# Kernel optimization log

Hardware: AMD Instinct MI355X
Metric: run time of the kernel (lower is better)

Reference implementation:

```python
import jax, jax.numpy as jnp
import numpy as np

NUM_ITERATIONS = 3


def squash(x, axis):
    # squared_norm/(1+squared_norm) * x / sqrt(squared_norm), as in the torch module
    sn = jnp.sum(x * x, axis=axis, keepdims=True)
    return sn / (1.0 + sn) * x / jnp.sqrt(sn)


def setup_inputs() -> dict:
    key = jax.random.key(0)
    k1, k2 = jax.random.split(key)
    batch, num_caps, num_route, in_ch, out_ch = 32, 32, 4608, 8, 16
    x = jax.random.normal(k1, (batch, num_route, in_ch), dtype=jnp.float32)
    route_weights = jax.random.normal(k2, (num_caps, num_route, in_ch, out_ch), dtype=jnp.float32)
    return {"x": x, "route_weights": route_weights}


def reference(x, route_weights):
    # U[b,c,r,1,o] = x[b,1,r,1,i] @ W[1,c,r,i,o]
    U = jnp.einsum("bri,crio->bcro", x, route_weights)[:, :, :, None, :]  # [b,c,r,1,o]
    B = jnp.zeros_like(U)
    V = None
    for _ in range(NUM_ITERATIONS):
        C = jax.nn.softmax(B, axis=1)                 # softmax over capsules
        S = jnp.sum(C * U, axis=2, keepdims=True)      # reduce over route nodes: [b,c,1,1,o]
        V = squash(S, axis=-1)
        B = B + U * V
    b, c = B.shape[0], B.shape[1]
    o = B.shape[-1]
    return V.reshape(b, c, o)
```

## Files before the change

kernel.cpp:

```cpp
#include <hip/hip_runtime.h>

#define BATCH 32
#define NCAPS 32
#define NR    4608
#define NI    8
#define NO    16
#define CSTR  200
#define MAXRB 36
#define NCH   256
#define L2E   1.44269504088896341f

typedef float f2 __attribute__((ext_vector_type(2)));
typedef _Float16 half4v __attribute__((ext_vector_type(4)));
typedef _Float16 half8v __attribute__((ext_vector_type(8)));

template<int RB>
__global__ __launch_bounds__(1024, 2) void caps_route_store(
    const float* __restrict__ x,
    const float* __restrict__ W,
    float* __restrict__ P,
    unsigned short* __restrict__ Uh)
{
    constexpr int NP = RB / 2;
    __shared__ __align__(16) float Ws[2][2][NCAPS * CSTR];
    __shared__ __align__(16) f2    xP[RB][8][2][NI];

    const int t  = threadIdx.x;
    const int om = (t & 3) | (((t >> 3) & 1) << 2);
    const int co = ((t >> 4) & 1) | (((t >> 2) & 1) << 1) | (((t >> 5) & 1) << 2);
    const int w  = t >> 6;
    const int oh = w & 1;
    const int bq = w >> 1;
    const int o  = oh * 8 + om;
    const int b0 = 4 * bq;
    const int r0 = blockIdx.x * RB;

    f2 acc[2][4];
#pragma unroll
    for (int p = 0; p < 2; ++p)
#pragma unroll
        for (int cl = 0; cl < 4; ++cl) acc[p][cl] = (f2)0.f;

    for (int s = t; s < RB * 16; s += 1024) {
        const int rr = s >> 4, bp = s & 15;
        const float* xp0 = &x[((size_t)(2 * bp + 0) * NR + r0 + rr) * NI];
        const float* xp1 = &x[((size_t)(2 * bp + 1) * NR + r0 + rr) * NI];
        const float4 a0 = *(const float4*)xp0;
        const float4 a1 = *(const float4*)(xp0 + 4);
        const float4 c0 = *(const float4*)xp1;
        const float4 c1 = *(const float4*)(xp1 + 4);
        f2* d = &xP[rr][bp >> 1][bp & 1][0];
        d[0] = f2{a0.x, c0.x}; d[1] = f2{a0.y, c0.y};
        d[2] = f2{a0.z, c0.z}; d[3] = f2{a0.w, c0.w};
        d[4] = f2{a1.x, c1.x}; d[5] = f2{a1.y, c1.y};
        d[6] = f2{a1.z, c1.z}; d[7] = f2{a1.w, c1.w};
    }

    const int c_st = t >> 5;
    const int sl   = (c_st >> 2) + 8 * (c_st & 3);
    const int part = t & 31;
    const int i_st = part >> 2;
    const int o0   = (part & 3) * 4;
    const int dst  = sl * CSTR + o0 * 12 + i_st;
    const float* wsrc = W + ((size_t)c_st * NR + r0) * (NI * NO) + part * 4;

    {
        const float4 s0 = *(const float4*)wsrc;
        const float4 s1 = *(const float4*)(wsrc + NI * NO);
        float* d0 = &Ws[0][0][dst];
        d0[0] = s0.x; d0[12] = s0.y; d0[24] = s0.z; d0[36] = s0.w;
        float* d1 = &Ws[0][1][dst];
        d1[0] = s1.x; d1[12] = s1.y; d1[24] = s1.z; d1[36] = s1.w;
    }
    float4 pfa = {}, pfb = {};
    if (NP > 1) {
        pfa = *(const float4*)(wsrc + 2 * NI * NO);
        pfb = *(const float4*)(wsrc + 3 * NI * NO);
    }
    __syncthreads();

    auto compute_store = [&](const float* wt, const f2* xv, int r) {
        f2 xq[2][NI];
#pragma unroll
        for (int i = 0; i < NI; ++i) { xq[0][i] = xv[i]; xq[1][i] = xv[NI + i]; }
        const float* wb = wt + co * CSTR + o * 12;
        f2 u[2][4];
#pragma unroll
        for (int cl = 0; cl < 4; ++cl) {
            const float* wp = wb + cl * (8 * CSTR);
            const float4 w0 = *(const float4*)wp;
            const float4 w1 = *(const float4*)(wp + 4);
#pragma unroll
            for (int p = 0; p < 2; ++p) {
                f2 u2 = xq[p][0] * w0.x;
                u2 += xq[p][1] * w0.y;
                u2 += xq[p][2] * w0.z;
                u2 += xq[p][3] * w0.w;
                u2 += xq[p][4] * w1.x;
                u2 += xq[p][5] * w1.y;
                u2 += xq[p][6] * w1.z;
                u2 += xq[p][7] * w1.w;
                u[p][cl] = u2;
                acc[p][cl] += u2;
            }
        }
        unsigned short* ub = Uh + (((size_t)r * BATCH + b0) * NO + o) * NCAPS + 4 * co;
#pragma unroll
        for (int bb = 0; bb < 4; ++bb) {
            const int p = bb >> 1, h = bb & 1;
            half4v hv;
            hv[0] = (_Float16)(h ? u[p][0].y : u[p][0].x);
            hv[1] = (_Float16)(h ? u[p][1].y : u[p][1].x);
            hv[2] = (_Float16)(h ? u[p][2].y : u[p][2].x);
            hv[3] = (_Float16)(h ? u[p][3].y : u[p][3].x);
            *(half4v*)(ub + (size_t)bb * (NO * NCAPS)) = hv;
        }
    };

#pragma unroll 1
    for (int rp = 0; rp < NP; ++rp) {
        const int cur = rp & 1;
        if (rp + 1 < NP) {
            float* d0 = &Ws[cur ^ 1][0][dst];
            d0[0] = pfa.x; d0[12] = pfa.y; d0[24] = pfa.z; d0[36] = pfa.w;
            float* d1 = &Ws[cur ^ 1][1][dst];
            d1[0] = pfb.x; d1[12] = pfb.y; d1[24] = pfb.z; d1[36] = pfb.w;
            if (rp + 2 < NP) {
                pfa = *(const float4*)(wsrc + (size_t)(2 * rp + 4) * (NI * NO));
                pfb = *(const float4*)(wsrc + (size_t)(2 * rp + 5) * (NI * NO));
            }
        }
        compute_store(&Ws[cur][0][0], &xP[2 * rp + 0][bq][0][0], r0 + 2 * rp + 0);
        compute_store(&Ws[cur][1][0], &xP[2 * rp + 1][bq][0][0], r0 + 2 * rp + 1);
        __syncthreads();
    }

#pragma unroll
    for (int bb = 0; bb < 4; ++bb) {
        const int p = bb >> 1, h = bb & 1;
        float* pout = P + (((size_t)blockIdx.x * BATCH + b0 + bb) * NO + o) * NCAPS + 4 * co;
        float4 v;
        v.x = (h ? acc[p][0].y : acc[p][0].x) * 0.03125f;
        v.y = (h ? acc[p][1].y : acc[p][1].x) * 0.03125f;
        v.z = (h ? acc[p][2].y : acc[p][2].x) * 0.03125f;
        v.w = (h ? acc[p][3].y : acc[p][3].x) * 0.03125f;
        *(float4*)pout = v;
    }
}

template<int RB>
__global__ __launch_bounds__(1024, 2) void caps_route_cached(
    const unsigned short* __restrict__ Uh,
    const float* __restrict__ A,
    float* __restrict__ P)
{
    const int t     = threadIdx.x;
    const int ch2   = t & 3;
    const int o     = (t >> 2) & 15;
    const int brel  = t >> 6;
    const int chunk = blockIdx.x >> 1;
    const int b     = 16 * (blockIdx.x & 1) + brel;
    const int r0    = chunk * RB;

    float a2[8];
#pragma unroll
    for (int cc = 0; cc < 8; ++cc)
        a2[cc] = A[(b * NCAPS + 8 * ch2 + cc) * NO + o] * L2E;
    float acc[8];
#pragma unroll
    for (int cc = 0; cc < 8; ++cc) acc[cc] = 0.f;

    const size_t S = (size_t)BATCH * NO * NCAPS;
    const unsigned short* up =
        Uh + (((size_t)r0 * BATCH + b) * NO + o) * NCAPS + 8 * ch2;

    uint4 q = *(const uint4*)up;
#pragma unroll 1
    for (int rr = 0; rr < RB; ++rr) {
        uint4 n = {};
        if (rr + 1 < RB) n = *(const uint4*)(up + S);
        up += S;

        const half8v h = __builtin_bit_cast(half8v, q);
        float Z = 0.f;
        float tt[8];
#pragma unroll
        for (int cc = 0; cc < 8; ++cc) {
            const float uu = (float)h[cc];
            const float ee = exp2f(uu * a2[cc]);
            Z += ee;
            tt[cc] = ee * uu;
        }
        Z += __shfl_xor(Z, 1);
        Z += __shfl_xor(Z, 2);
        const float rz = __builtin_amdgcn_rcpf(Z);
#pragma unroll
        for (int cc = 0; cc < 8; ++cc)
            acc[cc] = fmaf(tt[cc], rz, acc[cc]);

        q = n;
    }

    float* pout = P + (((size_t)chunk * BATCH + b) * NO + o) * NCAPS + 8 * ch2;
    float4 v0, v1;
    v0.x = acc[0]; v0.y = acc[1]; v0.z = acc[2]; v0.w = acc[3];
    v1.x = acc[4]; v1.y = acc[5]; v1.z = acc[6]; v1.w = acc[7];
    *(float4*)pout = v0;
    *(float4*)(pout + 4) = v1;
}

template<int RB, bool FIRST>
__global__ __launch_bounds__(1024, 2) void caps_route_fast(
    const float* __restrict__ x, const float* __restrict__ W,
    const float* __restrict__ A, float* __restrict__ P)
{
    constexpr int NP = RB / 2;
    __shared__ __align__(16) float Ws[2][2][NCAPS * CSTR];
    __shared__ __align__(16) f2    xP[RB][8][2][NI];

    const int t  = threadIdx.x;
    const int om = (t & 3) | (((t >> 3) & 1) << 2);
    const int co = ((t >> 4) & 1) | (((t >> 2) & 1) << 1) | (((t >> 5) & 1) << 2);
    const int w  = t >> 6;
    const int oh = w & 1;
    const int bq = w >> 1;
    const int o  = oh * 8 + om;
    const int b0 = 4 * bq;
    const int r0 = blockIdx.x * RB;

    f2 a2[2][4];
    if (!FIRST) {
#pragma unroll
        for (int p = 0; p < 2; ++p)
#pragma unroll
            for (int cl = 0; cl < 4; ++cl) {
                const int c = 4 * co + cl;
                a2[p][cl].x = A[((b0 + 2 * p + 0) * NCAPS + c) * NO + o] * L2E;
                a2[p][cl].y = A[((b0 + 2 * p + 1) * NCAPS + c) * NO + o] * L2E;
            }
    }
    f2 acc[2][4];
#pragma unroll
    for (int p = 0; p < 2; ++p)
#pragma unroll
        for (int cl = 0; cl < 4; ++cl) acc[p][cl] = (f2)0.f;

    for (int s = t; s < RB * 16; s += 1024) {
        const int rr = s >> 4, bp = s & 15;
        const float* xp0 = &x[((size_t)(2 * bp + 0) * NR + r0 + rr) * NI];
        const float* xp1 = &x[((size_t)(2 * bp + 1) * NR + r0 + rr) * NI];
        const float4 a0 = *(const float4*)xp0;
        const float4 a1 = *(const float4*)(xp0 + 4);
        const float4 c0 = *(const float4*)xp1;
        const float4 c1 = *(const float4*)(xp1 + 4);
        f2* d = &xP[rr][bp >> 1][bp & 1][0];
        d[0] = f2{a0.x, c0.x}; d[1] = f2{a0.y, c0.y};
        d[2] = f2{a0.z, c0.z}; d[3] = f2{a0.w, c0.w};
        d[4] = f2{a1.x, c1.x}; d[5] = f2{a1.y, c1.y};
        d[6] = f2{a1.z, c1.z}; d[7] = f2{a1.w, c1.w};
    }

    const int c_st = t >> 5;
    const int sl   = (c_st >> 2) + 8 * (c_st & 3);
    const int part = t & 31;
    const int i_st = part >> 2;
    const int o0   = (part & 3) * 4;
    const int dst  = sl * CSTR + o0 * 12 + i_st;
    const float* wsrc = W + ((size_t)c_st * NR + r0) * (NI * NO) + part * 4;

    {
        const float4 s0 = *(const float4*)wsrc;
        const float4 s1 = *(const float4*)(wsrc + NI * NO);
        float* d0 = &Ws[0][0][dst];
        d0[0] = s0.x; d0[12] = s0.y; d0[24] = s0.z; d0[36] = s0.w;
        float* d1 = &Ws[0][1][dst];
        d1[0] = s1.x; d1[12] = s1.y; d1[24] = s1.z; d1[36] = s1.w;
    }
    float4 pfa = {}, pfb = {};
    if (NP > 1) {
        pfa = *(const float4*)(wsrc + 2 * NI * NO);
        pfb = *(const float4*)(wsrc + 3 * NI * NO);
    }
    __syncthreads();

    auto compute_r = [&](const float* wt, const f2* xv) {
        f2 xq[2][NI];
#pragma unroll
        for (int i = 0; i < NI; ++i) { xq[0][i] = xv[i]; xq[1][i] = xv[NI + i]; }
        const float* wb = wt + co * CSTR + o * 12;
        if (FIRST) {
#pragma unroll
            for (int cl = 0; cl < 4; ++cl) {
                const float* wp = wb + cl * (8 * CSTR);
                const float4 w0 = *(const float4*)wp;
                const float4 w1 = *(const float4*)(wp + 4);
#pragma unroll
                for (int p = 0; p < 2; ++p) {
                    f2 u2 = xq[p][0] * w0.x;
                    u2 += xq[p][1] * w0.y;
                    u2 += xq[p][2] * w0.z;
                    u2 += xq[p][3] * w0.w;
                    u2 += xq[p][4] * w1.x;
                    u2 += xq[p][5] * w1.y;
                    u2 += xq[p][6] * w1.z;
                    u2 += xq[p][7] * w1.w;
                    acc[p][cl] += u2;
                }
            }
        } else {
            f2 tt[2][4];
            f2 Z0 = (f2)0.f, Z1 = (f2)0.f;
#pragma unroll
            for (int cl = 0; cl < 4; ++cl) {
                const float* wp = wb + cl * (8 * CSTR);
                const float4 w0 = *(const float4*)wp;
                const float4 w1 = *(const float4*)(wp + 4);
                f2 u0 = xq[0][0] * w0.x;
                u0 += xq[0][1] * w0.y;
                u0 += xq[0][2] * w0.z;
                u0 += xq[0][3] * w0.w;
                u0 += xq[0][4] * w1.x;
                u0 += xq[0][5] * w1.y;
                u0 += xq[0][6] * w1.z;
                u0 += xq[0][7] * w1.w;
                f2 u1 = xq[1][0] * w0.x;
                u1 += xq[1][1] * w0.y;
                u1 += xq[1][2] * w0.z;
                u1 += xq[1][3] * w0.w;
                u1 += xq[1][4] * w1.x;
                u1 += xq[1][5] * w1.y;
                u1 += xq[1][6] * w1.z;
                u1 += xq[1][7] * w1.w;
                const f2 l0 = u0 * a2[0][cl];
                const f2 l1 = u1 * a2[1][cl];
                f2 e0, e1;
                e0.x = exp2f(l0.x); e0.y = exp2f(l0.y);
                e1.x = exp2f(l1.x); e1.y = exp2f(l1.y);
                Z0 += e0; Z1 += e1;
                tt[0][cl] = e0 * u0;
                tt[1][cl] = e1 * u1;
            }
#pragma unroll
            for (int m = 0; m < 3; ++m) {
                const int msk = (m == 0) ? 4 : (m == 1) ? 16 : 32;
                Z0.x += __shfl_xor(Z0.x, msk); Z0.y += __shfl_xor(Z0.y, msk);
                Z1.x += __shfl_xor(Z1.x, msk); Z1.y += __shfl_xor(Z1.y, msk);
            }
            f2 rz0, rz1;
            rz0.x = __builtin_amdgcn_rcpf(Z0.x); rz0.y = __builtin_amdgcn_rcpf(Z0.y);
            rz1.x = __builtin_amdgcn_rcpf(Z1.x); rz1.y = __builtin_amdgcn_rcpf(Z1.y);
#pragma unroll
            for (int cl = 0; cl < 4; ++cl) {
                acc[0][cl] += tt[0][cl] * rz0;
                acc[1][cl] += tt[1][cl] * rz1;
            }
        }
    };

#pragma unroll 1
    for (int rp = 0; rp < NP; ++rp) {
        const int cur = rp & 1;
        if (rp + 1 < NP) {
            float* d0 = &Ws[cur ^ 1][0][dst];
            d0[0] = pfa.x; d0[12] = pfa.y; d0[24] = pfa.z; d0[36] = pfa.w;
            float* d1 = &Ws[cur ^ 1][1][dst];
            d1[0] = pfb.x; d1[12] = pfb.y; d1[24] = pfb.z; d1[36] = pfb.w;
            if (rp + 2 < NP) {
                pfa = *(const float4*)(wsrc + (size_t)(2 * rp + 4) * (NI * NO));
                pfb = *(const float4*)(wsrc + (size_t)(2 * rp + 5) * (NI * NO));
            }
        }
        compute_r(&Ws[cur][0][0], &xP[2 * rp + 0][bq][0][0]);
        compute_r(&Ws[cur][1][0], &xP[2 * rp + 1][bq][0][0]);
        __syncthreads();
    }

#pragma unroll
    for (int bb = 0; bb < 4; ++bb) {
        const int p = bb >> 1, h = bb & 1;
        float* pout = P + (((size_t)blockIdx.x * BATCH + b0 + bb) * NO + o) * NCAPS + 4 * co;
        float4 v;
        v.x = h ? acc[p][0].y : acc[p][0].x;
        v.y = h ? acc[p][1].y : acc[p][1].x;
        v.z = h ? acc[p][2].y : acc[p][2].x;
        v.w = h ? acc[p][3].y : acc[p][3].x;
        if (FIRST) { v.x *= 0.03125f; v.y *= 0.03125f; v.z *= 0.03125f; v.w *= 0.03125f; }
        *(float4*)pout = v;
    }
}

__global__ __launch_bounds__(256) void caps_partial(const float* __restrict__ P,
                                                    float* __restrict__ P2)
{
    const int tid = threadIdx.x;
    const int ct  = blockIdx.x & 15;
    const int rg  = blockIdx.x >> 4;
    const size_t col = (size_t)ct * 1024 + tid * 4;
    const float* p = P + (size_t)rg * 16 * 16384 + col;
    float4 s = {0.f, 0.f, 0.f, 0.f};
#pragma unroll
    for (int k = 0; k < 16; ++k) {
        const float4 v = *(const float4*)(p + (size_t)k * 16384);
        s.x += v.x; s.y += v.y; s.z += v.z; s.w += v.w;
    }
    *(float4*)(P2 + (size_t)rg * 16384 + col) = s;
}

__global__ void caps_reduce_squash(const float* __restrict__ P,
                                   float* __restrict__ A,
                                   float* __restrict__ out,
                                   int nchunk)
{
    __shared__ float sm[256];
    const int bc  = blockIdx.x;
    const int b   = bc >> 5;
    const int c   = bc & 31;
    const int tid = threadIdx.x;
    const int o = tid & 15;
    const int j = tid >> 4;
    float s = 0.f;
    for (int tch = j; tch < nchunk; tch += 16)
        s += P[(((size_t)tch * BATCH + b) * NO + o) * NCAPS + c];
    sm[tid] = s;
    __syncthreads();
    if (tid < 16) {
        float S = 0.f;
#pragma unroll
        for (int k = 0; k < 16; ++k) S += sm[tid + 16 * k];
        float sq = S * S;
#pragma unroll
        for (int d = 8; d >= 1; d >>= 1) sq += __shfl_xor(sq, d, 16);
        const float scale = sq / ((1.f + sq) * sqrtf(sq));
        const float V = S * scale;
        const int idx = bc * NO + tid;
        A[idx] += V;
        if (out) out[idx] = V;
    }
}

__global__ __launch_bounds__(512, 2) void caps_route_generic(
    const float* __restrict__ x, const float* __restrict__ W,
    const float* __restrict__ A, float* __restrict__ P, int rb)
{
    __shared__ __align__(16) float Ws[NCAPS * CSTR];
    __shared__ __align__(16) float xsT[NI * MAXRB * BATCH];

    const int t = threadIdx.x;
    const int b = t & 31;
    const int o = t >> 5;
    const int r0 = blockIdx.x * rb;
    const int rbs = rb * BATCH;

    float a2s[NCAPS];
#pragma unroll
    for (int c = 0; c < NCAPS; ++c)
        a2s[c] = A[(b * NCAPS + c) * NO + o] * L2E;
    float acc[NCAPS];
#pragma unroll
    for (int c = 0; c < NCAPS; ++c) acc[c] = 0.f;

    for (int s = t; s < rbs; s += 512) {
        const int rr = s >> 5, bb = s & 31;
        const float4 v0 = *(const float4*)&x[((size_t)bb * NR + r0 + rr) * NI];
        const float4 v1 = *(const float4*)&x[((size_t)bb * NR + r0 + rr) * NI + 4];
        const float tmp[8] = {v0.x, v0.y, v0.z, v0.w, v1.x, v1.y, v1.z, v1.w};
#pragma unroll
        for (int i = 0; i < NI; ++i) xsT[i * rbs + s] = tmp[i];
    }

    const int cs  = t >> 4;
    const int seg = t & 15;
    const int iw  = seg >> 1;
    const int ob  = (seg & 1) * 8;
    const float* wsrc = W + ((size_t)cs * NR + r0) * (NI * NO) + seg * 8;
    float4 pf0 = *(const float4*)wsrc;
    float4 pf1 = *(const float4*)(wsrc + 4);

    for (int rr = 0; rr < rb; ++rr) {
        __syncthreads();
        {
            const float tmp[8] = {pf0.x, pf0.y, pf0.z, pf0.w,
                                  pf1.x, pf1.y, pf1.z, pf1.w};
#pragma unroll
            for (int k = 0; k < 8; ++k)
                Ws[cs * CSTR + (ob + k) * 12 + iw] = tmp[k];
        }
        if (rr + 1 < rb) {
            wsrc += NI * NO;
            pf0 = *(const float4*)wsrc;
            pf1 = *(const float4*)(wsrc + 4);
        }
        __syncthreads();

        float xq[NI];
#pragma unroll
        for (int i = 0; i < NI; ++i) xq[i] = xsT[i * rbs + rr * 32 + b];

        float tt[NCAPS];
        float Z = 0.f;
        const float* bp2 = &Ws[o * 12];
#pragma unroll
        for (int c = 0; c < NCAPS; ++c) {
            const float* wp = bp2 + c * CSTR;
            const float4 w0 = *(const float4*)wp;
            const float4 w1 = *(const float4*)(wp + 4);
            float uu =      xq[0] * w0.x;
            uu = fmaf(xq[1], w0.y, uu);
            uu = fmaf(xq[2], w0.z, uu);
            uu = fmaf(xq[3], w0.w, uu);
            uu = fmaf(xq[4], w1.x, uu);
            uu = fmaf(xq[5], w1.y, uu);
            uu = fmaf(xq[6], w1.z, uu);
            uu = fmaf(xq[7], w1.w, uu);
            const float ee = exp2f(uu * a2s[c]);
            Z += ee;
            tt[c] = ee * uu;
        }
        const float rz = __builtin_amdgcn_rcpf(Z);
#pragma unroll
        for (int c = 0; c < NCAPS; ++c)
            acc[c] = fmaf(tt[c], rz, acc[c]);
    }

    float* pout = P + (((size_t)blockIdx.x * BATCH + b) * NO + o) * NCAPS;
#pragma unroll
    for (int q = 0; q < NCAPS / 4; ++q) {
        float4 v;
        v.x = acc[4 * q + 0]; v.y = acc[4 * q + 1];
        v.z = acc[4 * q + 2]; v.w = acc[4 * q + 3];
        *(float4*)(pout + 4 * q) = v;
    }
}

__global__ void caps_zero(float* __restrict__ p, int n)
{
    const int i = blockIdx.x * blockDim.x + threadIdx.x;
    if (i < n) p[i] = 0.f;
}

extern "C" void kernel_launch(void* const* d_in, const int* in_sizes, int n_in,
                              void* d_out, int out_size, void* d_ws, size_t ws_size,
                              hipStream_t stream)
{
    const float* x = (const float*)d_in[0];
    const float* W = (const float*)d_in[1];
    float* out = (float*)d_out;

    const size_t elem = (size_t)BATCH * NCAPS * NO;
    float* A  = (float*)d_ws;
    float* P  = A + elem;
    float* P2 = P + (size_t)NCH * elem;
    unsigned short* Uh = (unsigned short*)(P2 + 16 * elem);

    const size_t need_base = (size_t)(1 + NCH + 16) * elem * sizeof(float);
    const size_t need_u    = (size_t)NR * elem * sizeof(unsigned short);

    caps_zero<<<(int)((elem + 255) / 256), 256, 0, stream>>>(A, (int)elem);

    if (ws_size >= need_base + need_u) {
        caps_route_store<NR / NCH><<<NCH, 1024, 0, stream>>>(x, W, P, Uh);
        caps_partial<<<256, 256, 0, stream>>>(P, P2);
        caps_reduce_squash<<<BATCH * NCAPS, 256, 0, stream>>>(P2, A, nullptr, 16);
        caps_route_cached<NR / NCH><<<2 * NCH, 1024, 0, stream>>>(Uh, A, P);
        caps_partial<<<256, 256, 0, stream>>>(P, P2);
        caps_reduce_squash<<<BATCH * NCAPS, 256, 0, stream>>>(P2, A, nullptr, 16);
        caps_route_cached<NR / NCH><<<2 * NCH, 1024, 0, stream>>>(Uh, A, P);
        caps_partial<<<256, 256, 0, stream>>>(P, P2);
        caps_reduce_squash<<<BATCH * NCAPS, 256, 0, stream>>>(P2, A, out, 16);
    } else if (ws_size >= need_base) {
        caps_route_fast<NR / NCH, true><<<NCH, 1024, 0, stream>>>(x, W, A, P);
        caps_partial<<<256, 256, 0, stream>>>(P, P2);
        caps_reduce_squash<<<BATCH * NCAPS, 256, 0, stream>>>(P2, A, nullptr, 16);
        caps_route_fast<NR / NCH, false><<<NCH, 1024, 0, stream>>>(x, W, A, P);
        caps_partial<<<256, 256, 0, stream>>>(P, P2);
        caps_reduce_squash<<<BATCH * NCAPS, 256, 0, stream>>>(P2, A, nullptr, 16);
        caps_route_fast<NR / NCH, false><<<NCH, 1024, 0, stream>>>(x, W, A, P);
        caps_partial<<<256, 256, 0, stream>>>(P, P2);
        caps_reduce_squash<<<BATCH * NCAPS, 256, 0, stream>>>(P2, A, out, 16);
    } else {
        int nchunk = 128;
        while (nchunk > 32 &&
               (size_t)(nchunk + 1) * elem * sizeof(float) > ws_size)
            nchunk >>= 1;
        const int rb = NR / nchunk;
        for (int it = 0; it < 3; ++it) {
            caps_route_generic<<<nchunk, 512, 0, stream>>>(x, W, A, P, rb);
            caps_reduce_squash<<<BATCH * NCAPS, 256, 0, stream>>>(
                P, A, it == 2 ? out : nullptr, nchunk);
        }
    }
}
```

Baseline: 132.3 us.

## Compute U projection in store kernel with fp16 MFMA 32x32x8

Replaces the scalar FMA computation of U = x·W in the store kernel with a 32x32x8 f16 MFMA per route node and wave (one wave per output channel), re-laying out shared memory for x and W with padded strides to suit the MFMA operand fetch. Inputs are converted to fp16 before the multiply, which loses precision compared with fp32 math before the fp16 store of U. Uh and P outputs are now written as scalar 16-bit/32-bit stores rather than vectorized ones, and launch bounds drop to one block per SM.

```diff
diff --git a/kernel.cpp b/kernel.cpp
--- a/kernel.cpp
+++ b/kernel.cpp
@@ -6,6 +6,8 @@
 #define NI    8
 #define NO    16
 #define CSTR  200
+#define CSW   129
+#define CSX   9
 #define MAXRB 36
 #define NCH   256
 #define L2E   1.44269504088896341f
@@ -13,64 +15,48 @@
 typedef float f2 __attribute__((ext_vector_type(2)));
 typedef _Float16 half4v __attribute__((ext_vector_type(4)));
 typedef _Float16 half8v __attribute__((ext_vector_type(8)));
+typedef float f32x16 __attribute__((ext_vector_type(16)));
 
 template<int RB>
-__global__ __launch_bounds__(1024, 2) void caps_route_store(
+__global__ __launch_bounds__(1024, 1) void caps_route_store(
     const float* __restrict__ x,
     const float* __restrict__ W,
     float* __restrict__ P,
     unsigned short* __restrict__ Uh)
 {
     constexpr int NP = RB / 2;
-    __shared__ __align__(16) float Ws[2][2][NCAPS * CSTR];
-    __shared__ __align__(16) f2    xP[RB][8][2][NI];
-
-    const int t  = threadIdx.x;
-    const int om = (t & 3) | (((t >> 3) & 1) << 2);
-    const int co = ((t >> 4) & 1) | (((t >> 2) & 1) << 1) | (((t >> 5) & 1) << 2);
-    const int w  = t >> 6;
-    const int oh = w & 1;
-    const int bq = w >> 1;
-    const int o  = oh * 8 + om;
-    const int b0 = 4 * bq;
-    const int r0 = blockIdx.x * RB;
-
-    f2 acc[2][4];
-#pragma unroll
-    for (int p = 0; p < 2; ++p)
-#pragma unroll
-        for (int cl = 0; cl < 4; ++cl) acc[p][cl] = (f2)0.f;
-
-    for (int s = t; s < RB * 16; s += 1024) {
-        const int rr = s >> 4, bp = s & 15;
-        const float* xp0 = &x[((size_t)(2 * bp + 0) * NR + r0 + rr) * NI];
-        const float* xp1 = &x[((size_t)(2 * bp + 1) * NR + r0 + rr) * NI];
-        const float4 a0 = *(const float4*)xp0;
-        const float4 a1 = *(const float4*)(xp0 + 4);
-        const float4 c0 = *(const float4*)xp1;
-        const float4 c1 = *(const float4*)(xp1 + 4);
-        f2* d = &xP[rr][bp >> 1][bp & 1][0];
-        d[0] = f2{a0.x, c0.x}; d[1] = f2{a0.y, c0.y};
-        d[2] = f2{a0.z, c0.z}; d[3] = f2{a0.w, c0.w};
-        d[4] = f2{a1.x, c1.x}; d[5] = f2{a1.y, c1.y};
-        d[6] = f2{a1.z, c1.z}; d[7] = f2{a1.w, c1.w};
+    __shared__ __align__(16) float Ws2[2][2][NCAPS * CSW];
+    __shared__ __align__(16) float xQ[RB][BATCH * CSX];
+
+    const int t    = threadIdx.x;
+    const int lane = t & 63;
+    const int wv   = t >> 6;
+    const int cc   = lane & 31;
+    const int h    = lane >> 5;
+    const int r0   = blockIdx.x * RB;
+
+    for (int s = t; s < RB * BATCH; s += 1024) {
+        const int rr = s >> 5, b = s & 31;
+        const float* xp = &x[((size_t)b * NR + r0 + rr) * NI];
+        const float4 v0 = *(const float4*)xp;
+        const float4 v1 = *(const float4*)(xp + 4);
+        float* d = &xQ[rr][b * CSX];
+        d[0] = v0.x; d[1] = v0.y; d[2] = v0.z; d[3] = v0.w;
+        d[4] = v1.x; d[5] = v1.y; d[6] = v1.z; d[7] = v1.w;
     }
 
     const int c_st = t >> 5;
-    const int sl   = (c_st >> 2) + 8 * (c_st & 3);
     const int part = t & 31;
-    const int i_st = part >> 2;
-    const int o0   = (part & 3) * 4;
-    const int dst  = sl * CSTR + o0 * 12 + i_st;
+    const int dstw = c_st * CSW + part * 4;
     const float* wsrc = W + ((size_t)c_st * NR + r0) * (NI * NO) + part * 4;
 
     {
         const float4 s0 = *(const float4*)wsrc;
         const float4 s1 = *(const float4*)(wsrc + NI * NO);
-        float* d0 = &Ws[0][0][dst];
-        d0[0] = s0.x; d0[12] = s0.y; d0[24] = s0.z; d0[36] = s0.w;
-        float* d1 = &Ws[0][1][dst];
-        d1[0] = s1.x; d1[12] = s1.y; d1[24] = s1.z; d1[36] = s1.w;
+        float* d0 = &Ws2[0][0][dstw];
+        d0[0] = s0.x; d0[1] = s0.y; d0[2] = s0.z; d0[3] = s0.w;
+        float* d1 = &Ws2[0][1][dstw];
+        d1[0] = s1.x; d1[1] = s1.y; d1[2] = s1.z; d1[3] = s1.w;
     }
     float4 pfa = {}, pfb = {};
     if (NP > 1) {
@@ -79,72 +65,53 @@
     }
     __syncthreads();
 
-    auto compute_store = [&](const float* wt, const f2* xv, int r) {
-        f2 xq[2][NI];
-#pragma unroll
-        for (int i = 0; i < NI; ++i) { xq[0][i] = xv[i]; xq[1][i] = xv[NI + i]; }
-        const float* wb = wt + co * CSTR + o * 12;
-        f2 u[2][4];
-#pragma unroll
-        for (int cl = 0; cl < 4; ++cl) {
-            const float* wp = wb + cl * (8 * CSTR);
-            const float4 w0 = *(const float4*)wp;
-            const float4 w1 = *(const float4*)(wp + 4);
-#pragma unroll
-            for (int p = 0; p < 2; ++p) {
-                f2 u2 = xq[p][0] * w0.x;
-                u2 += xq[p][1] * w0.y;
-                u2 += xq[p][2] * w0.z;
-                u2 += xq[p][3] * w0.w;
-                u2 += xq[p][4] * w1.x;
-                u2 += xq[p][5] * w1.y;
-                u2 += xq[p][6] * w1.z;
-                u2 += xq[p][7] * w1.w;
-                u[p][cl] = u2;
-                acc[p][cl] += u2;
-            }
-        }
-        unsigned short* ub = Uh + (((size_t)r * BATCH + b0) * NO + o) * NCAPS + 4 * co;
-#pragma unroll
-        for (int bb = 0; bb < 4; ++bb) {
-            const int p = bb >> 1, h = bb & 1;
-            half4v hv;
-            hv[0] = (_Float16)(h ? u[p][0].y : u[p][0].x);
-            hv[1] = (_Float16)(h ? u[p][1].y : u[p][1].x);
-            hv[2] = (_Float16)(h ? u[p][2].y : u[p][2].x);
-            hv[3] = (_Float16)(h ? u[p][3].y : u[p][3].x);
-            *(half4v*)(ub + (size_t)bb * (NO * NCAPS)) = hv;
-        }
-    };
+    f32x16 acc = (f32x16)0.f;
+    const int xoff = cc * CSX + 4 * h;
+    const int woff = cc * CSW + 64 * h + wv;
+    unsigned short* ub0 = Uh + (size_t)r0 * (BATCH * NO * NCAPS) + wv * NCAPS + cc;
 
 #pragma unroll 1
     for (int rp = 0; rp < NP; ++rp) {
         const int cur = rp & 1;
         if (rp + 1 < NP) {
-            float* d0 = &Ws[cur ^ 1][0][dst];
-            d0[0] = pfa.x; d0[12] = pfa.y; d0[24] = pfa.z; d0[36] = pfa.w;
-            float* d1 = &Ws[cur ^ 1][1][dst];
-            d1[0] = pfb.x; d1[12] = pfb.y; d1[24] = pfb.z; d1[36] = pfb.w;
+            float* d0 = &Ws2[cur ^ 1][0][dstw];
+            d0[0] = pfa.x; d0[1] = pfa.y; d0[2] = pfa.z; d0[3] = pfa.w;
+            float* d1 = &Ws2[cur ^ 1][1][dstw];
+            d1[0] = pfb.x; d1[1] = pfb.y; d1[2] = pfb.z; d1[3] = pfb.w;
             if (rp + 2 < NP) {
                 pfa = *(const float4*)(wsrc + (size_t)(2 * rp + 4) * (NI * NO));
                 pfb = *(const float4*)(wsrc + (size_t)(2 * rp + 5) * (NI * NO));
             }
         }
-        compute_store(&Ws[cur][0][0], &xP[2 * rp + 0][bq][0][0], r0 + 2 * rp + 0);
-        compute_store(&Ws[cur][1][0], &xP[2 * rp + 1][bq][0][0], r0 + 2 * rp + 1);
+#pragma unroll
+        for (int sub = 0; sub < 2; ++sub) {
+            const int rr = 2 * rp + sub;
+            const float* xr = &xQ[rr][xoff];
+            const float* wr = &Ws2[cur][sub][woff];
+            half4v af, bf;
+            af[0] = (_Float16)xr[0]; af[1] = (_Float16)xr[1];
+            af[2] = (_Float16)xr[2]; af[3] = (_Float16)xr[3];
+            bf[0] = (_Float16)wr[0];  bf[1] = (_Float16)wr[16];
+            bf[2] = (_Float16)wr[32]; bf[3] = (_Float16)wr[48];
+            const f32x16 u =
+                __builtin_amdgcn_mfma_f32_32x32x8f16(af, bf, (f32x16)0.f, 0, 0, 0);
+            acc += u;
+            unsigned short* ub = ub0 + (size_t)rr * (BATCH * NO * NCAPS);
+#pragma unroll
+            for (int k = 0; k < 16; ++k) {
+                const int b = (k & 3) + 8 * (k >> 2) + 4 * h;
+                const _Float16 hv = (_Float16)u[k];
+                ub[(size_t)b * (NO * NCAPS)] = __builtin_bit_cast(unsigned short, hv);
+            }
+        }
         __syncthreads();
     }
 
-#pragma unroll
-    for (int bb = 0; bb < 4; ++bb) {
-        const int p = bb >> 1, h = bb & 1;
-        float* pout = P + (((size_t)blockIdx.x * BATCH + b0 + bb) * NO + o) * NCAPS + 4 * co;
-        float4 v;
-        v.x = (h ? acc[p][0].y : acc[p][0].x) * 0.03125f;
-        v.y = (h ? acc[p][1].y : acc[p][1].x) * 0.03125f;
-        v.z = (h ? acc[p][2].y : acc[p][2].x) * 0.03125f;
-        v.w = (h ? acc[p][3].y : acc[p][3].x) * 0.03125f;
-        *(float4*)pout = v;
+    float* pb = P + ((size_t)blockIdx.x * BATCH * NO + wv) * NCAPS + cc;
+#pragma unroll
+    for (int k = 0; k < 16; ++k) {
+        const int b = (k & 3) + 8 * (k >> 2) + 4 * h;
+        pb[(size_t)b * (NO * NCAPS)] = acc[k] * 0.03125f;
     }
 }
 
```

New measurement: 137.3 us. 3.8% more time.
